# Optimization experiments

Measured on AMD Instinct MI355X. Metric: run time of the kernel, lower is better.

## Reference

```python
import jax, jax.numpy as jnp
import numpy as np

N = 100000
E = 3200000
H = 4        # heads
C = 8        # hidden_dim per head
G = 512      # number of graphs
F_IN = 128
NEG_SLOPE = 0.2


def glorot(key, shape):
    fan = shape[0] + shape[-1]
    lim = jnp.sqrt(6.0 / fan)
    return jax.random.uniform(key, shape, jnp.float32, -lim, lim)


def setup_inputs() -> dict:
    key = jax.random.key(0)
    ks = jax.random.split(key, 32)
    x = jax.random.normal(ks[0], (N, F_IN), jnp.float32)
    edge_index = jax.random.randint(ks[1], (2, E), 0, N, jnp.int64)
    batch = jnp.sort(jax.random.randint(ks[2], (N,), 0, G, jnp.int64))
    d = {"x": x, "edge_index": edge_index, "batch": batch}
    in_dims = [F_IN, H * C, H * C, H * C]
    for i, din in enumerate(in_dims, start=1):
        d[f"W{i}"] = glorot(ks[3 + 4 * i], (din, H * C))
        d[f"as{i}"] = glorot(ks[4 + 4 * i], (H, C))
        d[f"ad{i}"] = glorot(ks[5 + 4 * i], (H, C))
        d[f"b{i}"] = jnp.zeros((H * C,), jnp.float32)
    d["fc_w"] = glorot(ks[30], (H * C, 1))
    d["fc_b"] = jnp.zeros((1,), jnp.float32)
    return d


def gat_layer(x, src, dst, W, a_src, a_dst, b):
    # x: [N, din]; src/dst: [E'] (with self-loops); returns [N, H*C]
    h = (x @ W).reshape(N, H, C)                         # [N,H,C]
    al_s = jnp.einsum('nhc,hc->nh', h, a_src)            # [N,H]
    al_d = jnp.einsum('nhc,hc->nh', h, a_dst)
    e = jax.nn.leaky_relu(al_s[src] + al_d[dst], NEG_SLOPE)  # [E',H]
    m = jax.ops.segment_max(e, dst, num_segments=N)      # [N,H]
    ee = jnp.exp(e - m[dst])
    denom = jax.ops.segment_sum(ee, dst, num_segments=N) # [N,H]
    alpha = ee / denom[dst]
    msg = alpha[:, :, None] * h[src]                     # [E',H,C]
    out = jax.ops.segment_sum(msg, dst, num_segments=N)  # [N,H,C]
    return out.reshape(N, H * C) + b


def reference(x, edge_index, batch, W1, as1, ad1, b1, W2, as2, ad2, b2,
              W3, as3, ad3, b3, W4, as4, ad4, b4, fc_w, fc_b):
    # PyG GATConv default: add self-loops
    loop = jnp.arange(N, dtype=edge_index.dtype)
    src = jnp.concatenate([edge_index[0], loop])
    dst = jnp.concatenate([edge_index[1], loop])
    h = jax.nn.elu(gat_layer(x, src, dst, W1, as1, ad1, b1))
    h = jax.nn.elu(gat_layer(h, src, dst, W2, as2, ad2, b2))
    h = jax.nn.elu(gat_layer(h, src, dst, W3, as3, ad3, b3))
    h = jax.nn.elu(gat_layer(h, src, dst, W4, as4, ad4, b4))
    # global mean pool over graphs
    sums = jax.ops.segment_sum(h, batch, num_segments=G)          # [G,HC]
    cnts = jax.ops.segment_sum(jnp.ones((N,), h.dtype), batch, num_segments=G)
    pooled = sums / jnp.maximum(cnts, 1.0)[:, None]
    return pooled @ fc_w + fc_b                                   # [G,1]
```

## Files before the change

### kernel.cpp

```cpp
#include <hip/hip_runtime.h>
#include <hip/hip_fp16.h>
#include <math.h>

#define NN 100000
#define NE 3200000
#define NHEAD 4
#define HC 32
#define NG 512
#define EDGES (NE + NN)

#define G1BLKS (NN / 8)

#define BKT_BITS 9
#define BKT_SIZE 512
#define NBKT 196
#define CHUNK1 16384
#define NB1 ((EDGES + CHUNK1 - 1) / CHUNK1)
#define CAP2 18432
#define PCHUNK 128

__device__ __forceinline__ float lrelu(float x) { return x > 0.f ? x : 0.2f * x; }

__global__ __launch_bounds__(256) void gemm1(
    const float* __restrict__ x, const float* __restrict__ W1,
    const float* __restrict__ as1, const float* __restrict__ ad1,
    __half* __restrict__ h, float* __restrict__ als, float* __restrict__ ald) {
    __shared__ float Wl[128 * HC];
    __shared__ float xl[8][128];
    int tid = threadIdx.x;
    for (int i = tid; i < 128 * HC; i += 256) Wl[i] = W1[i];
    int n0 = blockIdx.x * 8;
    {
        float4 v = *reinterpret_cast<const float4*>(x + n0 * 128 + tid * 4);
        int idx = tid * 4;
        int r = idx >> 7, c = idx & 127;
        *reinterpret_cast<float4*>(&xl[r][c]) = v;
    }
    __syncthreads();
    int r = tid >> 5, col = tid & 31;
    int n = n0 + r;
    float acc = 0.f;
#pragma unroll
    for (int k = 0; k < 128; ++k) acc = fmaf(xl[r][k], Wl[k * HC + col], acc);
    float s = acc * as1[col];
    float d = acc * ad1[col];
#pragma unroll
    for (int off = 1; off < 8; off <<= 1) {
        s += __shfl_xor(s, off);
        d += __shfl_xor(d, off);
    }
    h[n * HC + col] = __float2half(acc);
    if ((col & 7) == 0) {
        als[n * NHEAD + (col >> 3)] = s;
        ald[n * NHEAD + (col >> 3)] = d;
    }
}

__global__ __launch_bounds__(512) void pass1_hist(const int* __restrict__ ei,
                                                  int* __restrict__ Cmat) {
    __shared__ int hcnt[NBKT];
    for (int i = threadIdx.x; i < NBKT; i += 512) hcnt[i] = 0;
    __syncthreads();
    int base = blockIdx.x * CHUNK1;
    int lim = min(base + CHUNK1, EDGES);
    for (int e = base + threadIdx.x; e < lim; e += 512) {
        int dst = (e < NE) ? ei[NE + e] : (e - NE);
        atomicAdd(&hcnt[dst >> BKT_BITS], 1);
    }
    __syncthreads();
    int* row = Cmat + blockIdx.x * NBKT;
    for (int i = threadIdx.x; i < NBKT; i += 512) row[i] = hcnt[i];
}

__global__ __launch_bounds__(256) void bucket_scan(int* __restrict__ Cmat,
                                                   int* __restrict__ bucketStart) {
    __shared__ int tot[256];
    int k = threadIdx.x;
    int run = 0;
    if (k < NBKT) {
        for (int b = 0; b < NB1; ++b) {
            int idx = b * NBKT + k;
            int v = Cmat[idx];
            Cmat[idx] = run;
            run += v;
        }
    }
    tot[k] = (k < NBKT) ? run : 0;
    __syncthreads();
    int own = tot[k];
    for (int off = 1; off < 256; off <<= 1) {
        int u = (k >= off) ? tot[k - off] : 0;
        __syncthreads();
        tot[k] += u;
        __syncthreads();
    }
    if (k < NBKT) bucketStart[k] = tot[k] - own;
    if (k == 255) bucketStart[NBKT] = tot[255];
}

__global__ __launch_bounds__(512) void pass1_scatter(const int* __restrict__ ei,
                                                     const int* __restrict__ Cmat,
                                                     const int* __restrict__ bucketStart,
                                                     unsigned int* __restrict__ ebuf) {
    __shared__ int cur[NBKT];
    const int* row = Cmat + blockIdx.x * NBKT;
    for (int i = threadIdx.x; i < NBKT; i += 512) cur[i] = bucketStart[i] + row[i];
    __syncthreads();
    int base = blockIdx.x * CHUNK1;
    int lim = min(base + CHUNK1, EDGES);
    for (int e = base + threadIdx.x; e < lim; e += 512) {
        int src, dst;
        if (e < NE) { src = ei[e]; dst = ei[NE + e]; }
        else        { src = dst = e - NE; }
        int pos = atomicAdd(&cur[dst >> BKT_BITS], 1);
        ebuf[pos] = ((unsigned int)(dst & (BKT_SIZE - 1)) << 20) | (unsigned int)src;
    }
}

__global__ __launch_bounds__(1024) void pass2_sort(const unsigned int* __restrict__ ebuf,
                                                   const int* __restrict__ bucketStart,
                                                   int* __restrict__ csrsrc,
                                                   int* __restrict__ rowst) {
    __shared__ int hist[BKT_SIZE];
    __shared__ int scn[BKT_SIZE];
    __shared__ int staging[CAP2];
    int t = threadIdx.x;
    int k = blockIdx.x;
    int start = bucketStart[k], end = bucketStart[k + 1];
    int count = end - start;
    if (t < BKT_SIZE) hist[t] = 0;
    __syncthreads();
    for (int i = start + t; i < end; i += 1024)
        atomicAdd(&hist[ebuf[i] >> 20], 1);
    __syncthreads();
    if (t < BKT_SIZE) scn[t] = hist[t];
    __syncthreads();
    for (int off = 1; off < BKT_SIZE; off <<= 1) {
        int u = (t < BKT_SIZE && t >= off) ? scn[t - off] : 0;
        __syncthreads();
        if (t < BKT_SIZE) scn[t] += u;
        __syncthreads();
    }
    if (t < BKT_SIZE) {
        int ex = scn[t] - hist[t];
        rowst[k * BKT_SIZE + t] = start + ex;
        hist[t] = ex;
    }
    __syncthreads();
    for (int i = start + t; i < end; i += 1024) {
        unsigned int v = ebuf[i];
        int pos = atomicAdd(&hist[v >> 20], 1);
        if (pos < CAP2) staging[pos] = (int)(v & 0xFFFFFu);
    }
    __syncthreads();
    for (int i = t; i < count; i += 1024) csrsrc[start + i] = staging[i];
}

template<bool FUSE>
__global__ __launch_bounds__(256) void agg_layer(
    const int* __restrict__ rowst, const int* __restrict__ csrsrc,
    const float* __restrict__ als, const float* __restrict__ ald,
    const __half* __restrict__ h, const float* __restrict__ bias,
    const float* __restrict__ Wn, const float* __restrict__ asn,
    const float* __restrict__ adn,
    __half* __restrict__ h_out, float* __restrict__ als_out,
    float* __restrict__ ald_out, float* __restrict__ act_out) {
    __shared__ float Wl[HC * HC];
    int tid = threadIdx.x;
    if (FUSE) {
        for (int i = tid; i < HC * HC; i += 256) Wl[i] = Wn[i];
        __syncthreads();
    }
    int g = blockIdx.x * 8 + (tid >> 5);
    int lane = tid & 31;
    int head = lane >> 3;
    float adh = ald[g * NHEAD + head];
    int beg = rowst[g], end = (g + 1 < NN) ? rowst[g + 1] : EDGES;

    float acc0 = 0.f, acc1 = 0.f, acc2 = 0.f, acc3 = 0.f;
    float d0 = 0.f, d1 = 0.f, d2 = 0.f, d3 = 0.f;
    int k = beg;
    for (; k + 4 <= end; k += 4) {
        int s0 = csrsrc[k], s1 = csrsrc[k + 1], s2 = csrsrc[k + 2], s3 = csrsrc[k + 3];
        float p0 = __expf(lrelu(als[s0 * 4 + head] + adh));
        float p1 = __expf(lrelu(als[s1 * 4 + head] + adh));
        float p2 = __expf(lrelu(als[s2 * 4 + head] + adh));
        float p3 = __expf(lrelu(als[s3 * 4 + head] + adh));
        acc0 = fmaf(p0, __half2float(h[s0 * HC + lane]), acc0); d0 += p0;
        acc1 = fmaf(p1, __half2float(h[s1 * HC + lane]), acc1); d1 += p1;
        acc2 = fmaf(p2, __half2float(h[s2 * HC + lane]), acc2); d2 += p2;
        acc3 = fmaf(p3, __half2float(h[s3 * HC + lane]), acc3); d3 += p3;
    }
    for (; k < end; ++k) {
        int s = csrsrc[k];
        float p = __expf(lrelu(als[s * 4 + head] + adh));
        acc0 = fmaf(p, __half2float(h[s * HC + lane]), acc0); d0 += p;
    }
    float acc = (acc0 + acc1) + (acc2 + acc3);
    float d = (d0 + d1) + (d2 + d3);
    float v = acc / d + bias[lane];
    float av = v > 0.f ? v : (__expf(v) - 1.f);
    if (!FUSE) {
        act_out[g * HC + lane] = av;
        return;
    }
    float hacc = 0.f;
#pragma unroll
    for (int kk = 0; kk < HC; ++kk)
        hacc = fmaf(__shfl(av, kk, 32), Wl[kk * HC + lane], hacc);
    h_out[g * HC + lane] = __float2half(hacc);
    float sv = hacc * asn[lane];
    float dv = hacc * adn[lane];
#pragma unroll
    for (int off = 1; off < 8; off <<= 1) {
        sv += __shfl_xor(sv, off);
        dv += __shfl_xor(dv, off);
    }
    if ((lane & 7) == 0) {
        als_out[g * NHEAD + head] = sv;
        ald_out[g * NHEAD + head] = dv;
    }
}

__global__ void pool_init(float* __restrict__ sums, float* __restrict__ cnt) {
    int i = blockIdx.x * blockDim.x + threadIdx.x;
    if (i < NG * HC) sums[i] = 0.f;
    if (i < NG) cnt[i] = 0.f;
}

__global__ __launch_bounds__(256) void pool_seg(const float* __restrict__ act,
                                                const int* __restrict__ batch,
                                                float* __restrict__ sums,
                                                float* __restrict__ cnt) {
    int grp = blockIdx.x * 8 + (threadIdx.x >> 5);
    int lane = threadIdx.x & 31;
    int n0 = grp * PCHUNK;
    if (n0 >= NN) return;
    int n1 = min(n0 + PCHUNK, NN);
    int curg = batch[n0];
    float acc = 0.f, c = 0.f;
    for (int n = n0; n < n1; ++n) {
        int gg = batch[n];
        if (gg != curg) {
            atomicAdd(&sums[curg * HC + lane], acc);
            if (lane == 0) atomicAdd(&cnt[curg], c);
            acc = 0.f; c = 0.f; curg = gg;
        }
        acc += act[n * HC + lane];
        c += 1.f;
    }
    atomicAdd(&sums[curg * HC + lane], acc);
    if (lane == 0) atomicAdd(&cnt[curg], c);
}

__global__ void fc_out(const float* __restrict__ sums, const float* __restrict__ cnt,
                       const float* __restrict__ fcw, const float* __restrict__ fcb,
                       float* __restrict__ out) {
    int g = blockIdx.x;
    int lane = threadIdx.x;
    float v = (lane < HC) ? sums[g * HC + lane] * fcw[lane] : 0.f;
#pragma unroll
    for (int off = 32; off; off >>= 1) v += __shfl_down(v, off);
    if (lane == 0) out[g] = v / fmaxf(cnt[g], 1.f) + fcb[0];
}

extern "C" void kernel_launch(void* const* d_in, const int* in_sizes, int n_in,
                              void* d_out, int out_size, void* d_ws, size_t ws_size,
                              hipStream_t stream) {
    const float* x     = (const float*)d_in[0];
    const int*   ei    = (const int*)d_in[1];
    const int*   batch = (const int*)d_in[2];
    const float* W[4]   = {(const float*)d_in[3],  (const float*)d_in[7],
                           (const float*)d_in[11], (const float*)d_in[15]};
    const float* asr[4] = {(const float*)d_in[4],  (const float*)d_in[8],
                           (const float*)d_in[12], (const float*)d_in[16]};
    const float* adt[4] = {(const float*)d_in[5],  (const float*)d_in[9],
                           (const float*)d_in[13], (const float*)d_in[17]};
    const float* bb[4]  = {(const float*)d_in[6],  (const float*)d_in[10],
                           (const float*)d_in[14], (const float*)d_in[18]};
    const float* fcw = (const float*)d_in[19];
    const float* fcb = (const float*)d_in[20];
    float* out = (float*)d_out;

    char* ws = (char*)d_ws;
    size_t off = 0;
    auto carve = [&](size_t bytes) {
        void* p = ws + off;
        off += (bytes + 255) & ~size_t(255);
        return p;
    };
    __half* hA   = (__half*)carve(sizeof(__half) * NN * HC);
    __half* hB   = (__half*)carve(sizeof(__half) * NN * HC);
    float* actF  = (float*)carve(sizeof(float) * NN * HC);
    float* alsA  = (float*)carve(sizeof(float) * NN * NHEAD);
    float* aldA  = (float*)carve(sizeof(float) * NN * NHEAD);
    float* alsB  = (float*)carve(sizeof(float) * NN * NHEAD);
    float* aldB  = (float*)carve(sizeof(float) * NN * NHEAD);
    int*   Cmat  = (int*)carve(sizeof(int) * NB1 * NBKT);
    int*   bkst  = (int*)carve(sizeof(int) * (NBKT + 1));
    unsigned int* ebuf = (unsigned int*)carve(sizeof(unsigned int) * EDGES);
    int*   rowst = (int*)carve(sizeof(int) * NBKT * BKT_SIZE);
    int*   csrsrc= (int*)carve(sizeof(int) * EDGES);
    float* sums  = (float*)carve(sizeof(float) * NG * HC);
    float* cnt   = (float*)carve(sizeof(float) * NG);

    pass1_hist<<<NB1, 512, 0, stream>>>(ei, Cmat);
    bucket_scan<<<1, 256, 0, stream>>>(Cmat, bkst);
    pass1_scatter<<<NB1, 512, 0, stream>>>(ei, Cmat, bkst, ebuf);
    pass2_sort<<<NBKT, 1024, 0, stream>>>(ebuf, bkst, csrsrc, rowst);

    gemm1<<<G1BLKS, 256, 0, stream>>>(x, W[0], asr[0], adt[0], hA, alsA, aldA);

    agg_layer<true><<<G1BLKS, 256, 0, stream>>>(rowst, csrsrc, alsA, aldA, hA, bb[0],
                                                W[1], asr[1], adt[1],
                                                hB, alsB, aldB, nullptr);
    agg_layer<true><<<G1BLKS, 256, 0, stream>>>(rowst, csrsrc, alsB, aldB, hB, bb[1],
                                                W[2], asr[2], adt[2],
                                                hA, alsA, aldA, nullptr);
    agg_layer<true><<<G1BLKS, 256, 0, stream>>>(rowst, csrsrc, alsA, aldA, hA, bb[2],
                                                W[3], asr[3], adt[3],
                                                hB, alsB, aldB, nullptr);
    agg_layer<false><<<G1BLKS, 256, 0, stream>>>(rowst, csrsrc, alsB, aldB, hB, bb[3],
                                                 nullptr, nullptr, nullptr,
                                                 nullptr, nullptr, nullptr, actF);

    pool_init<<<(NG * HC + 255) / 256, 256, 0, stream>>>(sums, cnt);
    pool_seg<<<((NN + PCHUNK - 1) / PCHUNK + 7) / 8, 256, 0, stream>>>(actF, batch,
                                                                       sums, cnt);
    fc_out<<<NG, 64, 0, stream>>>(sums, cnt, fcw, fcb, out);
}
```

Before: 499.1 us.

## Parallelize bucket column scan and cooperatively compute edge weights in aggregation

The single-block serial bucket scan is replaced by a transposed count matrix, a per-bucket wavefront scan kernel and a small apex scan, so the column prefix sums run in parallel across many blocks. In the aggregation kernel, each group of 8 lanes now computes the attention exponent for 8 different edges at once and broadcasts weights and source indices via shuffles. This removes the 8x redundant exp/als loads per head that the old loop performed. The cost is more shuffles per edge, and the last chunk of each row does some wasted masked work. The kernel also reads rowst[g+1] for the last node, which relies on rowst being padded beyond NN entries.

```diff
diff --git a/kernel.cpp b/kernel.cpp
--- a/kernel.cpp
+++ b/kernel.cpp
@@ -16,6 +16,7 @@
 #define NBKT 196
 #define CHUNK1 16384
 #define NB1 ((EDGES + CHUNK1 - 1) / CHUNK1)
+#define NB1S 204
 #define CAP2 18432
 #define PCHUNK 128
 
@@ -57,7 +58,7 @@
 }
 
 __global__ __launch_bounds__(512) void pass1_hist(const int* __restrict__ ei,
-                                                  int* __restrict__ Cmat) {
+                                                  int* __restrict__ CmatT) {
     __shared__ int hcnt[NBKT];
     for (int i = threadIdx.x; i < NBKT; i += 512) hcnt[i] = 0;
     __syncthreads();
@@ -68,26 +69,43 @@
         atomicAdd(&hcnt[dst >> BKT_BITS], 1);
     }
     __syncthreads();
-    int* row = Cmat + blockIdx.x * NBKT;
-    for (int i = threadIdx.x; i < NBKT; i += 512) row[i] = hcnt[i];
-}
-
-__global__ __launch_bounds__(256) void bucket_scan(int* __restrict__ Cmat,
+    for (int i = threadIdx.x; i < NBKT; i += 512)
+        CmatT[i * NB1S + blockIdx.x] = hcnt[i];
+}
+
+__global__ __launch_bounds__(64) void colscan2(int* __restrict__ CmatT,
+                                               int* __restrict__ degTot) {
+    int k = blockIdx.x;
+    int lane = threadIdx.x;
+    int* p = CmatT + k * NB1S;
+    int i0 = lane * 4;
+    int v0 = (i0 + 0 < NB1) ? p[i0 + 0] : 0;
+    int v1 = (i0 + 1 < NB1) ? p[i0 + 1] : 0;
+    int v2 = (i0 + 2 < NB1) ? p[i0 + 2] : 0;
+    int v3 = (i0 + 3 < NB1) ? p[i0 + 3] : 0;
+    int e1 = v0, e2 = v0 + v1, e3 = v0 + v1 + v2;
+    int tot = e3 + v3;
+    int run = tot;
+#pragma unroll
+    for (int off = 1; off < 64; off <<= 1) {
+        int u = __shfl_up(run, off);
+        if (lane >= off) run += u;
+    }
+    int excl = run - tot;
+    if (i0 + 0 < NB1) p[i0 + 0] = excl;
+    if (i0 + 1 < NB1) p[i0 + 1] = excl + e1;
+    if (i0 + 2 < NB1) p[i0 + 2] = excl + e2;
+    if (i0 + 3 < NB1) p[i0 + 3] = excl + e3;
+    if (lane == 63) degTot[k] = run;
+}
+
+__global__ __launch_bounds__(256) void bucket_apex(const int* __restrict__ degTot,
                                                    int* __restrict__ bucketStart) {
     __shared__ int tot[256];
     int k = threadIdx.x;
-    int run = 0;
-    if (k < NBKT) {
-        for (int b = 0; b < NB1; ++b) {
-            int idx = b * NBKT + k;
-            int v = Cmat[idx];
-            Cmat[idx] = run;
-            run += v;
-        }
-    }
-    tot[k] = (k < NBKT) ? run : 0;
-    __syncthreads();
-    int own = tot[k];
+    int own = (k < NBKT) ? degTot[k] : 0;
+    tot[k] = own;
+    __syncthreads();
     for (int off = 1; off < 256; off <<= 1) {
         int u = (k >= off) ? tot[k - off] : 0;
         __syncthreads();
@@ -99,12 +117,12 @@
 }
 
 __global__ __launch_bounds__(512) void pass1_scatter(const int* __restrict__ ei,
-                                                     const int* __restrict__ Cmat,
+                                                     const int* __restrict__ CmatT,
                                                      const int* __restrict__ bucketStart,
                                                      unsigned int* __restrict__ ebuf) {
     __shared__ int cur[NBKT];
-    const int* row = Cmat + blockIdx.x * NBKT;
-    for (int i = threadIdx.x; i < NBKT; i += 512) cur[i] = bucketStart[i] + row[i];
+    for (int i = threadIdx.x; i < NBKT; i += 512)
+        cur[i] = bucketStart[i] + CmatT[i * NB1S + blockIdx.x];
     __syncthreads();
     int base = blockIdx.x * CHUNK1;
     int lim = min(base + CHUNK1, EDGES);
@@ -174,31 +192,36 @@
     int g = blockIdx.x * 8 + (tid >> 5);
     int lane = tid & 31;
     int head = lane >> 3;
+    int slot = lane & 7;
     float adh = ald[g * NHEAD + head];
-    int beg = rowst[g], end = (g + 1 < NN) ? rowst[g + 1] : EDGES;
-
-    float acc0 = 0.f, acc1 = 0.f, acc2 = 0.f, acc3 = 0.f;
-    float d0 = 0.f, d1 = 0.f, d2 = 0.f, d3 = 0.f;
-    int k = beg;
-    for (; k + 4 <= end; k += 4) {
-        int s0 = csrsrc[k], s1 = csrsrc[k + 1], s2 = csrsrc[k + 2], s3 = csrsrc[k + 3];
-        float p0 = __expf(lrelu(als[s0 * 4 + head] + adh));
-        float p1 = __expf(lrelu(als[s1 * 4 + head] + adh));
-        float p2 = __expf(lrelu(als[s2 * 4 + head] + adh));
-        float p3 = __expf(lrelu(als[s3 * 4 + head] + adh));
-        acc0 = fmaf(p0, __half2float(h[s0 * HC + lane]), acc0); d0 += p0;
-        acc1 = fmaf(p1, __half2float(h[s1 * HC + lane]), acc1); d1 += p1;
-        acc2 = fmaf(p2, __half2float(h[s2 * HC + lane]), acc2); d2 += p2;
-        acc3 = fmaf(p3, __half2float(h[s3 * HC + lane]), acc3); d3 += p3;
-    }
-    for (; k < end; ++k) {
-        int s = csrsrc[k];
-        float p = __expf(lrelu(als[s * 4 + head] + adh));
-        acc0 = fmaf(p, __half2float(h[s * HC + lane]), acc0); d0 += p;
-    }
-    float acc = (acc0 + acc1) + (acc2 + acc3);
-    float d = (d0 + d1) + (d2 + d3);
-    float v = acc / d + bias[lane];
+    int beg = rowst[g], end = rowst[g + 1];
+
+    float acc[8];
+#pragma unroll
+    for (int j = 0; j < 8; ++j) acc[j] = 0.f;
+    float dsum = 0.f;
+    const __half* hL = h + lane;
+
+    for (int c0 = beg; c0 < end; c0 += 8) {
+        int e = c0 + slot;
+        int s = (e < end) ? csrsrc[e] : 0;
+        float p = __expf(lrelu(als[s * NHEAD + head] + adh));
+        p = (e < end) ? p : 0.f;
+        dsum += p;
+#pragma unroll
+        for (int j = 0; j < 8; ++j) {
+            float pj = __shfl(p, (head << 3) | j, 32);
+            int sj = __shfl(s, j, 32);
+            acc[j] = fmaf(pj, __half2float(hL[sj * HC]), acc[j]);
+        }
+    }
+    float a = ((acc[0] + acc[1]) + (acc[2] + acc[3])) +
+              ((acc[4] + acc[5]) + (acc[6] + acc[7]));
+    dsum += __shfl_xor(dsum, 1, 32);
+    dsum += __shfl_xor(dsum, 2, 32);
+    dsum += __shfl_xor(dsum, 4, 32);
+
+    float v = a / dsum + bias[lane];
     float av = v > 0.f ? v : (__expf(v) - 1.f);
     if (!FUSE) {
         act_out[g * HC + lane] = av;
@@ -296,7 +319,8 @@
     float* aldA  = (float*)carve(sizeof(float) * NN * NHEAD);
     float* alsB  = (float*)carve(sizeof(float) * NN * NHEAD);
     float* aldB  = (float*)carve(sizeof(float) * NN * NHEAD);
-    int*   Cmat  = (int*)carve(sizeof(int) * NB1 * NBKT);
+    int*   CmatT = (int*)carve(sizeof(int) * NBKT * NB1S);
+    int*   degTot= (int*)carve(sizeof(int) * NBKT);
     int*   bkst  = (int*)carve(sizeof(int) * (NBKT + 1));
     unsigned int* ebuf = (unsigned int*)carve(sizeof(unsigned int) * EDGES);
     int*   rowst = (int*)carve(sizeof(int) * NBKT * BKT_SIZE);
@@ -304,9 +328,10 @@
     float* sums  = (float*)carve(sizeof(float) * NG * HC);
     float* cnt   = (float*)carve(sizeof(float) * NG);
 
-    pass1_hist<<<NB1, 512, 0, stream>>>(ei, Cmat);
-    bucket_scan<<<1, 256, 0, stream>>>(Cmat, bkst);
-    pass1_scatter<<<NB1, 512, 0, stream>>>(ei, Cmat, bkst, ebuf);
+    pass1_hist<<<NB1, 512, 0, stream>>>(ei, CmatT);
+    colscan2<<<NBKT, 64, 0, stream>>>(CmatT, degTot);
+    bucket_apex<<<1, 256, 0, stream>>>(degTot, bkst);
+    pass1_scatter<<<NB1, 512, 0, stream>>>(ei, CmatT, bkst, ebuf);
     pass2_sort<<<NBKT, 1024, 0, stream>>>(ebuf, bkst, csrsrc, rowst);
 
     gemm1<<<G1BLKS, 256, 0, stream>>>(x, W[0], asr[0], adt[0], hA, alsA, aldA);
```

New measurement: 444.6 us. 1.12x faster.
